# Performance work log

Measured on AMD Instinct MI355X. Metric: run time of the kernel, lower is better.

## Reference

```python
import jax, jax.numpy as jnp
import numpy as np

N = 5
C = 256
B, H, W = 8, 64, 64


def setup_inputs() -> dict:
    key = jax.random.key(0)
    ks = jax.random.split(key, 9)
    s = 0.05
    return {
        "inputs": jax.random.normal(ks[0], (B, N, C, H, W), dtype=jnp.float32),
        # grouped 1x1 conv: groups = N-1, each group maps C channels -> 1 channel, no bias
        "wgt_w": jax.random.normal(ks[1], (N - 1, C), dtype=jnp.float32) * s,
        # ConvGRU 1x1 gate convs: in = 2*C (cat of input and hidden), out = C, with bias
        "w_r": jax.random.normal(ks[2], (C, 2 * C), dtype=jnp.float32) * s,
        "b_r": jnp.zeros((C,), dtype=jnp.float32),
        "w_u": jax.random.normal(ks[3], (C, 2 * C), dtype=jnp.float32) * s,
        "b_u": jnp.zeros((C,), dtype=jnp.float32),
        "w_o": jax.random.normal(ks[4], (C, 2 * C), dtype=jnp.float32) * s,
        "b_o": jnp.zeros((C,), dtype=jnp.float32),
        "gamma": jax.random.normal(ks[5], (1,), dtype=jnp.float32) * s,
    }


def _conv1x1(x, Wm, bias):
    # x: [b, cin, h, w]; Wm: [cout, cin]
    return jnp.einsum("bchw,oc->bohw", x, Wm) + bias[None, :, None, None]


def reference(inputs, wgt_w, w_r, b_r, w_u, b_u, w_o, b_o, gamma):
    b, n, c, h, w = inputs.shape

    def gru(x, hprev):
        s = jnp.concatenate([x, hprev], axis=1)  # [b, 2c, h, w]
        u = jax.nn.sigmoid(_conv1x1(s, w_u, b_u))
        r = jax.nn.sigmoid(_conv1x1(s, w_r, b_r))
        o = jnp.tanh(_conv1x1(jnp.concatenate([x, hprev * r], axis=1), w_o, b_o))
        return hprev * (1.0 - u) + o * u

    preds = []
    for i in range(n):
        h_t = inputs[:, i]  # [b, c, h, w]
        idx = [j for j in range(n) if j != i]
        h_n = inputs[:, jnp.array(idx)]  # [b, n-1, c, h, w], neighbor-major channel layout
        diff = h_t[:, None] - h_n  # repeat(h_t, n-1) - cat(neighbors)
        # grouped 1x1 conv (groups = n-1, no bias): per-neighbor channel reduction
        wgt = jnp.einsum("bjchw,jc->bjhw", diff, wgt_w)  # [b, n-1, h, w]
        gate = jax.nn.sigmoid(wgt)
        # torch: wgt.unsqueeze(1).repeat(1, c, 1, 1, 1).view(b, c*(n-1), h, w)
        # -> flat channel index = cc*(n-1) + j  (note: differs from x2's j*c + cc layout)
        gate_full = jnp.broadcast_to(gate[:, None], (b, c, n - 1, h, w)).reshape(
            b, c * (n - 1), h, w
        )
        x2 = h_n.reshape(b, (n - 1) * c, h, w)
        msg = x2 * gate_full
        m_t = msg.reshape(b, n - 1, c, h, w).sum(axis=1)  # sum-aggregate over neighbors
        h_new = gru(m_t, h_t)
        preds.append(h_new * gamma + h_t)
    return jnp.stack(preds, axis=1)  # [b, n, c, h, w]
```

## Files before the change

### kernel.cpp

```cpp
#include <hip/hip_runtime.h>

typedef __attribute__((ext_vector_type(8))) short short8;
typedef __attribute__((ext_vector_type(4))) float f32x4;
typedef __attribute__((ext_vector_type(8))) unsigned short us8;
typedef __attribute__((ext_vector_type(4))) unsigned short us4;
typedef __attribute__((ext_vector_type(2))) unsigned short us2;

__device__ __forceinline__ float sigmoidf_(float x){ return 1.f/(1.f+__expf(-x)); }
__device__ __forceinline__ unsigned short f2bf(float f){
    union{float f; unsigned int u;} x; x.f = f;
    unsigned int r = x.u + 0x7fffu + ((x.u>>16)&1u);
    return (unsigned short)(r>>16);
}
__device__ __forceinline__ float bf2f(unsigned short u){
    union{unsigned int u; float f;} x; x.u = ((unsigned int)u)<<16; return x.f;
}
#define GAS(p) ((const __attribute__((address_space(1))) void*)(uintptr_t)(p))
#define LAS(p) ((__attribute__((address_space(3))) void*)(uintptr_t)(p))

#define SLOT 8388608ull

__global__ __launch_bounds__(256) void k_wp2(const float* __restrict__ w_u, const float* __restrict__ w_r,
                                             const float* __restrict__ w_o,
                                             unsigned short* __restrict__ Wc0, unsigned short* __restrict__ Wc1){
    int bx = blockIdx.x;
    const float *s0, *s1; unsigned short* dst; int OCN, tid;
    if (bx < 256){ tid = bx*256 + threadIdx.x; OCN = 512; s0 = w_u; s1 = w_r; dst = Wc0; }
    else         { tid = (bx-256)*256 + threadIdx.x; OCN = 256; s0 = w_o; s1 = w_o; dst = Wc1; }
    int d = tid*4;
    int kk = d & 63;
    int row = d >> 6;
    int oc = row & (OCN-1);
    int kb = row / OCN;
    int k  = kb*64 + kk;
    const float* src = (oc < 256) ? s0 : s1;
    int ocr = (oc < 256) ? oc : oc-256;
    float4 v = *(const float4*)&src[(size_t)ocr*512 + k];
    us4 pk; pk.x=f2bf(v.x); pk.y=f2bf(v.y); pk.z=f2bf(v.z); pk.w=f2bf(v.w);
    int kk_sw = kk ^ ((oc&7)<<3);
    *(us4*)&dst[(size_t)row*64 + kk_sw] = pk;
}

__global__ __launch_bounds__(256) void k_bxsd(const float* __restrict__ inp, const float* __restrict__ wgt,
                                              unsigned short* __restrict__ Alo, unsigned short* __restrict__ Ahi,
                                              int i0, int cnt){
    __shared__ float wg[1024];
    __shared__ float dpart[8*640];
    __shared__ float Dl[640];
    __shared__ unsigned short tm[64*34];
    __shared__ unsigned short th[64*34];
    int t  = threadIdx.x;
    int p0 = blockIdx.x << 5;
    int b  = p0 >> 12, pl0 = p0 & 4095;
    for (int s=t; s<1024; s+=256) wg[s] = wgt[s];
    __syncthreads();
    {
        int px = t & 31, cg = t >> 5;
        float d[20];
        #pragma unroll
        for (int o=0;o<20;o++) d[o]=0.f;
        #pragma unroll
        for (int cc=0; cc<32; cc++){
            int c = cg*32 + cc;
            float w0 = wg[c], w1 = wg[256+c], w2 = wg[512+c], w3 = wg[768+c];
            #pragma unroll
            for (int n=0;n<5;n++){
                float v = inp[(((size_t)((b*5+n)*256+c))<<12) + pl0 + px];
                d[n*4+0] += v*w0; d[n*4+1] += v*w1; d[n*4+2] += v*w2; d[n*4+3] += v*w3;
            }
        }
        #pragma unroll
        for (int o=0;o<20;o++) dpart[cg*640 + o*32 + px] = d[o];
    }
    __syncthreads();
    for (int o=t; o<640; o+=256){
        float s = 0.f;
        #pragma unroll
        for (int g=0; g<8; g++) s += dpart[g*640 + o];
        Dl[o] = s;
    }
    __syncthreads();
    for (int ct=0; ct<4; ct++){
        int c0 = ct << 6;
        f32x4 x[5][2], S4[2];
        #pragma unroll
        for (int q=0;q<2;q++){
            int s = t + q*256;
            int c = s >> 3, pc = (s&7) << 2;
            int cc = c0 + c;
            f32x4 acc = {0.f,0.f,0.f,0.f};
            #pragma unroll
            for (int n=0;n<5;n++){
                x[n][q] = *(const f32x4*)&inp[(((size_t)((b*5+n)*256+cc))<<12) + pl0 + pc];
                acc += x[n][q];
            }
            S4[q] = acc;
        }
        #pragma unroll
        for (int i=0;i<5;i++){
            if (i < i0 || i >= i0+cnt) continue;
            #pragma unroll
            for (int q=0;q<2;q++){
                int s = t + q*256;
                int c = s >> 3, pc = (s&7) << 2;
                int j = c & 3;
                int node = (j < i) ? j : (j+1);
                f32x4 dw = *(const f32x4*)&Dl[(i*4+j)*32 + pc];
                f32x4 dn = *(const f32x4*)&Dl[(node*4+j)*32 + pc];
                f32x4 xi = x[i][q];
                f32x4 md = S4[q] - xi;
                int lb = c*34 + pc;
                us2 m0, m1, h0, h1;
                m0.x = f2bf(sigmoidf_(dw.x-dn.x)*md.x); m0.y = f2bf(sigmoidf_(dw.y-dn.y)*md.y);
                m1.x = f2bf(sigmoidf_(dw.z-dn.z)*md.z); m1.y = f2bf(sigmoidf_(dw.w-dn.w)*md.w);
                h0.x = f2bf(xi.x); h0.y = f2bf(xi.y); h1.x = f2bf(xi.z); h1.y = f2bf(xi.w);
                *(us2*)&tm[lb] = m0; *(us2*)&tm[lb+2] = m1;
                *(us2*)&th[lb] = h0; *(us2*)&th[lb+2] = h1;
            }
            __syncthreads();
            {
                int p = t >> 3, cs = (t&7) << 3;
                us8 vm, vh;
                #pragma unroll
                for (int j8=0;j8<8;j8++){ vm[j8] = tm[(cs+j8)*34 + p]; vh[j8] = th[(cs+j8)*34 + p]; }
                int cs_sw = cs ^ ((p&7)<<3);
                size_t dst = (size_t)(i - i0)*SLOT + ((size_t)ct*32768 + p0 + p)*64 + cs_sw;
                *(us8*)&Alo[dst] = vm;
                *(us8*)&Ahi[dst] = vh;
            }
            __syncthreads();
        }
    }
}

template<int EPI>
__global__ __launch_bounds__(256) void k_mm(
        const unsigned short* __restrict__ Alo, const unsigned short* __restrict__ Ahi,
        const unsigned short* __restrict__ Wb,
        const float* __restrict__ inp, const float* __restrict__ b0, const float* __restrict__ b1,
        unsigned short* __restrict__ U, unsigned short* __restrict__ A1hi, float* __restrict__ outp,
        const float* __restrict__ gamma_p, int i0, int cnt)
{
    constexpr int OCN = EPI ? 256 : 512;
    constexpr int NY  = EPI ? 2   : 4;
    __shared__ unsigned short As[3][128*64];
    __shared__ unsigned short Bs[3][128*64];
    int t  = threadIdx.x, wv = t>>6, ln = t&63;
    int NU = 256*NY*cnt;
    int NS = (NU >> 8) * 8;
    int chunk = blockIdx.x >> 5, k_in = blockIdx.x & 31;
    int ubase = chunk*(NU>>3) + k_in;
    int oc0 = (ubase & (NY-1)) * 128;
    int wm = (wv>>1)*64, wn = (wv&1)*64;
    int row = ln & 15, quad = ln >> 4, kq = quad*8;
    int rsw = (row&7)<<3;
    float gm = EPI ? gamma_p[0] : 0.f;

    f32x4 acc[4][4];
    f32x4 zr = {0.f,0.f,0.f,0.f};
    #pragma unroll
    for (int a=0;a<4;a++){
        #pragma unroll
        for (int o=0;o<4;o++) acc[a][o]=zr;
    }

    auto stage = [&](int s){
        if (s >= NS) return;
        int u  = ubase + (s>>3)*32;
        int pz = u / NY;
        int kb = s & 7;
        int p0s = (pz & 255) << 7;
        size_t zos = (size_t)(pz >> 8) * SLOT;
        const unsigned short* gA = (kb<4) ? (Alo + zos + ((size_t)kb*32768 + p0s)*64)
                                          : (Ahi + zos + ((size_t)(kb-4)*32768 + p0s)*64);
        const unsigned short* gW = Wb + ((size_t)kb*OCN + oc0)*64;
        int buf = s % 3;
        #pragma unroll
        for (int q=0;q<4;q++){
            int off = (wv*4+q)*512;
            __builtin_amdgcn_global_load_lds(GAS(gA + off + ln*8), LAS(&Bs[buf][off + ln*8]), 16, 0, 0);
            __builtin_amdgcn_global_load_lds(GAS(gW + off + ln*8), LAS(&As[buf][off + ln*8]), 16, 0, 0);
        }
    };

    stage(0); stage(1);
    for (int s=0; s<NS; ++s){
        if (s+1 < NS) { asm volatile("s_waitcnt vmcnt(8)" ::: "memory"); }
        else          { asm volatile("s_waitcnt vmcnt(0)" ::: "memory"); }
        __builtin_amdgcn_s_barrier();
        __builtin_amdgcn_sched_barrier(0);
        stage(s+2);
        const int cur = s % 3;
        #pragma unroll
        for (int ks=0; ks<2; ks++){
            short8 a[4], b[4];
            int col = (ks*32 + kq) ^ rsw;
            #pragma unroll
            for (int f=0; f<4; f++){
                a[f] = *(const short8*)&As[cur][(wm+f*16+row)*64 + col];
                b[f] = *(const short8*)&Bs[cur][(wn+f*16+row)*64 + col];
            }
            #pragma unroll
            for (int fm=0; fm<4; fm++){
                #pragma unroll
                for (int fn=0; fn<4; fn++)
                    acc[fm][fn] = __builtin_amdgcn_mfma_f32_16x16x32_bf16(a[fm], b[fn], acc[fm][fn], 0,0,0);
            }
        }
        if ((s&7)==7){
            int u  = ubase + (s>>3)*32;
            int pz = u / NY;
            int p0 = (pz & 255) << 7;
            int z  = pz >> 8;
            size_t zo = (size_t)z*SLOT;
            int i  = i0 + z;
            if (EPI==0){
                if (oc0 < 256){
                    size_t ub = zo + (size_t)((p0>>7)*2 + (oc0>>7))*16384 + (size_t)t*4;
                    #pragma unroll
                    for (int fn=0; fn<4; fn++){
                        #pragma unroll
                        for (int fm=0; fm<4; fm++){
                            int ocb = oc0 + wm + fm*16 + quad*4;
                            us4 pk;
                            #pragma unroll
                            for (int r=0;r<4;r++)
                                pk[r] = f2bf(sigmoidf_(acc[fm][fn][r] + b0[ocb+r]));
                            *(us4*)&U[ub + (size_t)(fn*4+fm)*1024] = pk;
                        }
                    }
                } else {
                    #pragma unroll
                    for (int fn=0; fn<4; fn++){
                        int p = p0 + wn + fn*16 + row;
                        #pragma unroll
                        for (int fm=0; fm<4; fm++){
                            int ocb = oc0 + wm + fm*16 + quad*4;
                            int kb2 = ocb - 256;
                            int kc  = (kb2&63) ^ ((p&7)<<3);
                            size_t aidx = zo + ((size_t)(kb2>>6)*32768 + p)*64 + kc;
                            us4 vh = *(const us4*)&Ahi[aidx];
                            us4 pk;
                            #pragma unroll
                            for (int r=0;r<4;r++){
                                float rg = sigmoidf_(acc[fm][fn][r] + b1[kb2+r]);
                                pk[r] = f2bf(rg * bf2f(vh[r]));
                            }
                            *(us4*)&A1hi[aidx] = pk;
                        }
                    }
                }
            } else {
                size_t ub = zo + (size_t)((p0>>7)*2 + (oc0>>7))*16384 + (size_t)t*4;
                #pragma unroll
                for (int fn=0; fn<4; fn++){
                    int p  = p0 + wn + fn*16 + row;
                    int b  = p >> 12, pl = p & 4095;
                    size_t hb = (((size_t)((b*5+i)*256))<<12) + pl;
                    #pragma unroll
                    for (int fm=0; fm<4; fm++){
                        int ocb = oc0 + wm + fm*16 + quad*4;
                        us4 vu = *(const us4*)&U[ub + (size_t)(fn*4+fm)*1024];
                        #pragma unroll
                        for (int r=0;r<4;r++){
                            int oc = ocb + r;
                            float v  = acc[fm][fn][r] + b0[oc];
                            float e2 = __expf(2.f*v);
                            float thv = 1.f - 2.f/(e2+1.f);
                            float uu = bf2f(vu[r]);
                            float h  = inp[hb + ((size_t)oc<<12)];
                            float hn = h*(1.f-uu) + thv*uu;
                            outp[hb + ((size_t)oc<<12)] = hn*gm + h;
                        }
                    }
                }
            }
            #pragma unroll
            for (int a2=0;a2<4;a2++){
                #pragma unroll
                for (int o2=0;o2<4;o2++) acc[a2][o2]=zr;
            }
        }
    }
}

extern "C" void kernel_launch(void* const* d_in, const int* in_sizes, int n_in,
                              void* d_out, int out_size, void* d_ws, size_t ws_size,
                              hipStream_t stream) {
    const float* inputs = (const float*)d_in[0];
    const float* wgt_w  = (const float*)d_in[1];
    const float* w_r    = (const float*)d_in[2];
    const float* b_r    = (const float*)d_in[3];
    const float* w_u    = (const float*)d_in[4];
    const float* b_u    = (const float*)d_in[5];
    const float* w_o    = (const float*)d_in[6];
    const float* b_o    = (const float*)d_in[7];
    const float* gamma  = (const float*)d_in[8];
    float* out = (float*)d_out;

    unsigned short* Wc0 = (unsigned short*)d_ws;
    unsigned short* Wc1 = Wc0 + 262144;
    unsigned short* U   = Wc1 + 131072;

    size_t fixedB = (262144ull + 131072ull)*2;
    size_t slotB  = 4ull*SLOT*2;
    int nb = 1;
    for (int k2=5;k2>=1;k2--){ if (fixedB + (size_t)k2*slotB <= ws_size){ nb = k2; break; } }

    unsigned short* Alo  = U   + (size_t)nb*SLOT;
    unsigned short* Ahi  = Alo + (size_t)nb*SLOT;
    unsigned short* A1hi = Ahi + (size_t)nb*SLOT;

    k_wp2 <<<384, 256, 0, stream>>>(w_u, w_r, w_o, Wc0, Wc1);
    for (int i0=0; i0<5; i0+=nb){
        int cnt = (5-i0 < nb) ? (5-i0) : nb;
        k_bxsd<<<1024, 256, 0, stream>>>(inputs, wgt_w, Alo, Ahi, i0, cnt);
        k_mm<0><<<256, 256, 0, stream>>>(Alo, Ahi, Wc0, inputs, b_u, b_r,
                                         U, A1hi, nullptr, gamma, i0, cnt);
        k_mm<1><<<256, 256, 0, stream>>>(Alo, A1hi, Wc1, inputs, b_o, nullptr,
                                         U, nullptr, out, gamma, i0, cnt);
    }
}
```

Baseline: 753.5 us.

## Enlarge GEMM tiles to 256x256 with 512-thread blocks and non-persistent grid

Replaces the persistent 128x128-tile GEMM with one 256x256 output tile per 512-thread block, launched over a 3D grid with the slot index in z. It moves to a double-buffered LDS pipeline with syncthreads and raises MFMA wave priority during compute. The U buffer layout is changed to 256-pixel tiles to match. This aims to increase operand reuse per LDS byte. In exchange, the 128 KB of LDS likely limits occupancy to one block per CU, and the pipeline is shallower.

```diff
diff --git a/kernel.cpp b/kernel.cpp
--- a/kernel.cpp
+++ b/kernel.cpp
@@ -134,151 +134,137 @@
 }
 
 template<int EPI>
-__global__ __launch_bounds__(256) void k_mm(
+__global__ __launch_bounds__(512,2) void k_mm(
         const unsigned short* __restrict__ Alo, const unsigned short* __restrict__ Ahi,
         const unsigned short* __restrict__ Wb,
         const float* __restrict__ inp, const float* __restrict__ b0, const float* __restrict__ b1,
         unsigned short* __restrict__ U, unsigned short* __restrict__ A1hi, float* __restrict__ outp,
-        const float* __restrict__ gamma_p, int i0, int cnt)
+        const float* __restrict__ gamma_p, int i0)
 {
     constexpr int OCN = EPI ? 256 : 512;
-    constexpr int NY  = EPI ? 2   : 4;
-    __shared__ unsigned short As[3][128*64];
-    __shared__ unsigned short Bs[3][128*64];
+    constexpr int NY  = EPI ? 1   : 2;
+    constexpr int NWG = 128*NY;
+    __shared__ unsigned short As[2][256*64];
+    __shared__ unsigned short Bs[2][256*64];
     int t  = threadIdx.x, wv = t>>6, ln = t&63;
-    int NU = 256*NY*cnt;
-    int NS = (NU >> 8) * 8;
-    int chunk = blockIdx.x >> 5, k_in = blockIdx.x & 31;
-    int ubase = chunk*(NU>>3) + k_in;
-    int oc0 = (ubase & (NY-1)) * 128;
-    int wm = (wv>>1)*64, wn = (wv&1)*64;
+
+    int bid = blockIdx.x;
+    int wg  = (bid&7)*(NWG>>3) + (bid>>3);
+    int oc0 = (wg & (NY-1)) * 256;
+    int p0  = (wg / NY) * 256;
+
+    int z  = blockIdx.z, i = i0 + z;
+    size_t zo = (size_t)z*SLOT;
+    int wm = (wv>>2)*128, wn = (wv&3)*64;
     int row = ln & 15, quad = ln >> 4, kq = quad*8;
-    int rsw = (row&7)<<3;
-    float gm = EPI ? gamma_p[0] : 0.f;
-
-    f32x4 acc[4][4];
+
+    f32x4 acc[8][4];
     f32x4 zr = {0.f,0.f,0.f,0.f};
     #pragma unroll
-    for (int a=0;a<4;a++){
+    for (int a=0;a<8;a++){
         #pragma unroll
         for (int o=0;o<4;o++) acc[a][o]=zr;
     }
 
-    auto stage = [&](int s){
-        if (s >= NS) return;
-        int u  = ubase + (s>>3)*32;
-        int pz = u / NY;
-        int kb = s & 7;
-        int p0s = (pz & 255) << 7;
-        size_t zos = (size_t)(pz >> 8) * SLOT;
-        const unsigned short* gA = (kb<4) ? (Alo + zos + ((size_t)kb*32768 + p0s)*64)
-                                          : (Ahi + zos + ((size_t)(kb-4)*32768 + p0s)*64);
+    auto stage = [&](int kb, int buf){
+        const unsigned short* gA = (kb<4) ? (Alo + zo + ((size_t)kb*32768 + p0)*64)
+                                          : (Ahi + zo + ((size_t)(kb-4)*32768 + p0)*64);
         const unsigned short* gW = Wb + ((size_t)kb*OCN + oc0)*64;
-        int buf = s % 3;
         #pragma unroll
         for (int q=0;q<4;q++){
-            int off = (wv*4+q)*512;
-            __builtin_amdgcn_global_load_lds(GAS(gA + off + ln*8), LAS(&Bs[buf][off + ln*8]), 16, 0, 0);
-            __builtin_amdgcn_global_load_lds(GAS(gW + off + ln*8), LAS(&As[buf][off + ln*8]), 16, 0, 0);
+            int idx = (q*512 + t)*8;
+            __builtin_amdgcn_global_load_lds(GAS(gA + idx), LAS(&Bs[buf][idx]), 16, 0, 0);
+            __builtin_amdgcn_global_load_lds(GAS(gW + idx), LAS(&As[buf][idx]), 16, 0, 0);
         }
     };
 
-    stage(0); stage(1);
-    for (int s=0; s<NS; ++s){
-        if (s+1 < NS) { asm volatile("s_waitcnt vmcnt(8)" ::: "memory"); }
-        else          { asm volatile("s_waitcnt vmcnt(0)" ::: "memory"); }
-        __builtin_amdgcn_s_barrier();
-        __builtin_amdgcn_sched_barrier(0);
-        stage(s+2);
-        const int cur = s % 3;
+    stage(0, 0);
+    __syncthreads();
+
+    int rsw = (row&7)<<3;
+    for (int kb=0; kb<8; ++kb){
+        const int cur = kb & 1;
+        if (kb < 7) stage(kb+1, cur^1);
         #pragma unroll
         for (int ks=0; ks<2; ks++){
-            short8 a[4], b[4];
+            short8 a[8], b[4];
             int col = (ks*32 + kq) ^ rsw;
             #pragma unroll
-            for (int f=0; f<4; f++){
+            for (int f=0; f<8; f++)
                 a[f] = *(const short8*)&As[cur][(wm+f*16+row)*64 + col];
+            #pragma unroll
+            for (int f=0; f<4; f++)
                 b[f] = *(const short8*)&Bs[cur][(wn+f*16+row)*64 + col];
-            }
-            #pragma unroll
-            for (int fm=0; fm<4; fm++){
+            __builtin_amdgcn_s_setprio(1);
+            #pragma unroll
+            for (int fm=0; fm<8; fm++){
                 #pragma unroll
                 for (int fn=0; fn<4; fn++)
                     acc[fm][fn] = __builtin_amdgcn_mfma_f32_16x16x32_bf16(a[fm], b[fn], acc[fm][fn], 0,0,0);
             }
-        }
-        if ((s&7)==7){
-            int u  = ubase + (s>>3)*32;
-            int pz = u / NY;
-            int p0 = (pz & 255) << 7;
-            int z  = pz >> 8;
-            size_t zo = (size_t)z*SLOT;
-            int i  = i0 + z;
-            if (EPI==0){
-                if (oc0 < 256){
-                    size_t ub = zo + (size_t)((p0>>7)*2 + (oc0>>7))*16384 + (size_t)t*4;
+            __builtin_amdgcn_s_setprio(0);
+        }
+        __syncthreads();
+    }
+
+    if (EPI==0){
+        if (oc0 == 0){
+            size_t ub = zo + (size_t)(p0>>8)*65536 + (size_t)t*4;
+            #pragma unroll
+            for (int fn=0; fn<4; fn++){
+                #pragma unroll
+                for (int fm=0; fm<8; fm++){
+                    int ocb = wm + fm*16 + quad*4;
+                    us4 pk;
                     #pragma unroll
-                    for (int fn=0; fn<4; fn++){
-                        #pragma unroll
-                        for (int fm=0; fm<4; fm++){
-                            int ocb = oc0 + wm + fm*16 + quad*4;
-                            us4 pk;
-                            #pragma unroll
-                            for (int r=0;r<4;r++)
-                                pk[r] = f2bf(sigmoidf_(acc[fm][fn][r] + b0[ocb+r]));
-                            *(us4*)&U[ub + (size_t)(fn*4+fm)*1024] = pk;
-                        }
+                    for (int r=0;r<4;r++)
+                        pk[r] = f2bf(sigmoidf_(acc[fm][fn][r] + b0[ocb+r]));
+                    *(us4*)&U[ub + (size_t)(fn*8+fm)*2048] = pk;
+                }
+            }
+        } else {
+            #pragma unroll
+            for (int fn=0; fn<4; fn++){
+                int p = p0 + wn + fn*16 + row;
+                int psw = (p&7)<<3;
+                #pragma unroll
+                for (int fm=0; fm<8; fm++){
+                    int kb2 = wm + fm*16 + quad*4;
+                    size_t aidx = zo + ((size_t)(kb2>>6)*32768 + p)*64 + ((kb2&63)^psw);
+                    us4 vh = *(const us4*)&Ahi[aidx];
+                    us4 pk;
+                    #pragma unroll
+                    for (int r=0;r<4;r++){
+                        float rg = sigmoidf_(acc[fm][fn][r] + b1[kb2+r]);
+                        pk[r] = f2bf(rg * bf2f(vh[r]));
                     }
-                } else {
-                    #pragma unroll
-                    for (int fn=0; fn<4; fn++){
-                        int p = p0 + wn + fn*16 + row;
-                        #pragma unroll
-                        for (int fm=0; fm<4; fm++){
-                            int ocb = oc0 + wm + fm*16 + quad*4;
-                            int kb2 = ocb - 256;
-                            int kc  = (kb2&63) ^ ((p&7)<<3);
-                            size_t aidx = zo + ((size_t)(kb2>>6)*32768 + p)*64 + kc;
-                            us4 vh = *(const us4*)&Ahi[aidx];
-                            us4 pk;
-                            #pragma unroll
-                            for (int r=0;r<4;r++){
-                                float rg = sigmoidf_(acc[fm][fn][r] + b1[kb2+r]);
-                                pk[r] = f2bf(rg * bf2f(vh[r]));
-                            }
-                            *(us4*)&A1hi[aidx] = pk;
-                        }
-                    }
+                    *(us4*)&A1hi[aidx] = pk;
                 }
-            } else {
-                size_t ub = zo + (size_t)((p0>>7)*2 + (oc0>>7))*16384 + (size_t)t*4;
-                #pragma unroll
-                for (int fn=0; fn<4; fn++){
-                    int p  = p0 + wn + fn*16 + row;
-                    int b  = p >> 12, pl = p & 4095;
-                    size_t hb = (((size_t)((b*5+i)*256))<<12) + pl;
-                    #pragma unroll
-                    for (int fm=0; fm<4; fm++){
-                        int ocb = oc0 + wm + fm*16 + quad*4;
-                        us4 vu = *(const us4*)&U[ub + (size_t)(fn*4+fm)*1024];
-                        #pragma unroll
-                        for (int r=0;r<4;r++){
-                            int oc = ocb + r;
-                            float v  = acc[fm][fn][r] + b0[oc];
-                            float e2 = __expf(2.f*v);
-                            float thv = 1.f - 2.f/(e2+1.f);
-                            float uu = bf2f(vu[r]);
-                            float h  = inp[hb + ((size_t)oc<<12)];
-                            float hn = h*(1.f-uu) + thv*uu;
-                            outp[hb + ((size_t)oc<<12)] = hn*gm + h;
-                        }
-                    }
+            }
+        }
+    } else {
+        float gm = gamma_p[0];
+        size_t ub = zo + (size_t)(p0>>8)*65536 + (size_t)t*4;
+        #pragma unroll
+        for (int fn=0; fn<4; fn++){
+            int p  = p0 + wn + fn*16 + row;
+            int b  = p >> 12, pl = p & 4095;
+            size_t hb = (((size_t)((b*5+i)*256))<<12) + pl;
+            #pragma unroll
+            for (int fm=0; fm<8; fm++){
+                int ocb = wm + fm*16 + quad*4;
+                us4 vu = *(const us4*)&U[ub + (size_t)(fn*8+fm)*2048];
+                #pragma unroll
+                for (int r=0;r<4;r++){
+                    int oc = ocb + r;
+                    float v  = acc[fm][fn][r] + b0[oc];
+                    float e2 = __expf(2.f*v);
+                    float thv = 1.f - 2.f/(e2+1.f);
+                    float uu = bf2f(vu[r]);
+                    float h  = inp[hb + ((size_t)oc<<12)];
+                    float hn = h*(1.f-uu) + thv*uu;
+                    outp[hb + ((size_t)oc<<12)] = hn*gm + h;
                 }
-            }
-            #pragma unroll
-            for (int a2=0;a2<4;a2++){
-                #pragma unroll
-                for (int o2=0;o2<4;o2++) acc[a2][o2]=zr;
             }
         }
     }
@@ -315,9 +301,9 @@
     for (int i0=0; i0<5; i0+=nb){
         int cnt = (5-i0 < nb) ? (5-i0) : nb;
         k_bxsd<<<1024, 256, 0, stream>>>(inputs, wgt_w, Alo, Ahi, i0, cnt);
-        k_mm<0><<<256, 256, 0, stream>>>(Alo, Ahi, Wc0, inputs, b_u, b_r,
-                                         U, A1hi, nullptr, gamma, i0, cnt);
-        k_mm<1><<<256, 256, 0, stream>>>(Alo, A1hi, Wc1, inputs, b_o, nullptr,
-                                         U, nullptr, out, gamma, i0, cnt);
-    }
-}
+        k_mm<0><<<dim3(256,1,cnt), 512, 0, stream>>>(Alo, Ahi, Wc0, inputs, b_u, b_r,
+                                                     U, A1hi, nullptr, gamma, i0);
+        k_mm<1><<<dim3(128,1,cnt), 512, 0, stream>>>(Alo, A1hi, Wc1, inputs, b_o, nullptr,
+                                                     U, nullptr, out, gamma, i0);
+    }
+}
```

New measurement: 865.2 us. 14.8% more time.
